# Performance work log

Hardware: AMD Instinct MI355X
Metric: run time of the kernel (lower is better)

Reference implementation:

```python
import jax, jax.numpy as jnp
import numpy as np

N, E, F_IN, F_E = 50000, 800000, 128, 16
R, H, C = 4, 4, 32            # num_relations, heads, out_channels
HC = H * C                     # 128
NEG_SLOPE = 0.2                # PyG RGATConv default negative_slope
EPS = 1e-16                    # PyG softmax epsilon


def rgat_conv(x, src, dst, edge_type, edge_attr, w, q, k, e, le, b, concat):
    """Faithful PyG RGATConv (additive-self-attention, across-relation, dim=1, aggr=add).
    x: [N,F]; w: [R,F,H*C]; q,k,e: [H*C,H]; le: [F_e,H*C]; b: bias."""
    n = x.shape[0]
    xw = jnp.einsum('nf,rfo->rno', x, w)              # [R,N,H*C] per-relation projections
    x_i = xw[edge_type, dst]                          # [E,H*C] target-node proj per edge
    x_j = xw[edge_type, src]                          # [E,H*C] source-node proj per edge
    qi = x_i @ q                                      # [E,H]
    kj = x_j @ k + (edge_attr @ le) @ e               # [E,H] (edge features folded into keys)
    alpha = jax.nn.leaky_relu(qi + kj, NEG_SLOPE)     # [E,H]
    # softmax over incoming edges of each destination node (across relations)
    amax = jax.ops.segment_max(alpha, dst, num_segments=n)
    ex = jnp.exp(alpha - amax[dst])
    denom = jax.ops.segment_sum(ex, dst, num_segments=n)
    alpha = ex / (denom[dst] + EPS)
    msg = alpha[:, :, None] * x_j.reshape(-1, H, C)   # [E,H,C]
    out = jax.ops.segment_sum(msg, dst, num_segments=n)  # [N,H,C] sum aggregation
    out = out.reshape(n, H * C) if concat else out.mean(axis=1)
    return out + b


def setup_inputs() -> dict:
    key = jax.random.key(0)
    ks = jax.random.split(key, 18)
    p = 0.05
    inp = {
        'x': jax.random.normal(ks[0], (N, F_IN), dtype=jnp.float32),
        'edge_index': jax.random.randint(ks[1], (2, E), 0, N, dtype=jnp.int64)
            if jax.config.jax_enable_x64 else jax.random.randint(ks[1], (2, E), 0, N).astype(jnp.int32),
        'edge_attr': jax.random.normal(ks[2], (E, F_E), dtype=jnp.float32),
        'edge_type': jax.random.randint(ks[3], (E,), 0, R).astype(jnp.int32),
        # conv1 params (in=F_IN, concat=True -> bias of size H*C)
        'w1': jax.random.normal(ks[4], (R, F_IN, HC), dtype=jnp.float32) * p,
        'q1': jax.random.normal(ks[5], (HC, H), dtype=jnp.float32) * p,
        'k1': jax.random.normal(ks[6], (HC, H), dtype=jnp.float32) * p,
        'e1': jax.random.normal(ks[7], (HC, H), dtype=jnp.float32) * p,
        'le1': jax.random.normal(ks[8], (F_E, HC), dtype=jnp.float32) * p,
        'b1': jnp.zeros((HC,), dtype=jnp.float32),
        # conv3 params (in=H*C=128, concat=False -> bias of size C)
        'w3': jax.random.normal(ks[9], (R, HC, HC), dtype=jnp.float32) * p,
        'q3': jax.random.normal(ks[10], (HC, H), dtype=jnp.float32) * p,
        'k3': jax.random.normal(ks[11], (HC, H), dtype=jnp.float32) * p,
        'e3': jax.random.normal(ks[12], (HC, H), dtype=jnp.float32) * p,
        'le3': jax.random.normal(ks[13], (F_E, HC), dtype=jnp.float32) * p,
        'b3': jnp.zeros((C,), dtype=jnp.float32),
    }
    return inp


def reference(x, edge_index, edge_attr, edge_type,
              w1, q1, k1, e1, le1, b1,
              w3, q3, k3, e3, le3, b3):
    src, dst = edge_index[0], edge_index[1]
    h = jax.nn.relu(rgat_conv(x, src, dst, edge_type, edge_attr,
                              w1, q1, k1, e1, le1, b1, concat=True))
    out = rgat_conv(h, src, dst, edge_type, edge_attr,
                    w3, q3, k3, e3, le3, b3, concat=False)
    return out
```

## Files before the change

### kernel.cpp

```cpp
#include <hip/hip_runtime.h>


#define NEG_SLOPE 0.2f
#define SOFT_EPS 1e-16f

typedef __attribute__((ext_vector_type(8))) short bf16x8;
typedef __attribute__((ext_vector_type(4))) float f32x4;
typedef __attribute__((ext_vector_type(4))) unsigned short u16x4;
typedef __attribute__((ext_vector_type(4))) _Float16 half4;
typedef __attribute__((ext_vector_type(8))) _Float16 half8;

__device__ __forceinline__ void bf16split(float f, unsigned short& h, unsigned short& l) {
  unsigned u = __float_as_uint(f);
  unsigned r = u + 0x7FFFu + ((u >> 16) & 1u);
  h = (unsigned short)(r >> 16);
  float fh = __uint_as_float(((unsigned)h) << 16);
  float d = f - fh;
  unsigned u2 = __float_as_uint(d);
  unsigned r2 = u2 + 0x7FFFu + ((u2 >> 16) & 1u);
  l = (unsigned short)(r2 >> 16);
}

__global__ void lee_kernel(const float* __restrict__ le1, const float* __restrict__ e1,
                           const float* __restrict__ le3, const float* __restrict__ e3,
                           float* __restrict__ lee) {
  int t = threadIdx.x;
  const float* le = (t < 64) ? le1 : le3;
  const float* ee = (t < 64) ? e1 : e3;
  int u = t & 63, f = u >> 2, h = u & 3;
  float acc = 0.f;
  for (int o = 0; o < 128; ++o) acc += le[f * 128 + o] * ee[o * 4 + h];
  lee[t] = acc;
}

__global__ __launch_bounds__(256) void wqk_kernel(
    const float* __restrict__ w1, const float* __restrict__ q1, const float* __restrict__ k1,
    const float* __restrict__ w3, const float* __restrict__ q3, const float* __restrict__ k3,
    float* __restrict__ wqk) {
  int idx = blockIdx.x * 256 + threadIdx.x;
  int L = idx >> 12, rem = idx & 4095;
  int r = rem >> 10, rem2 = rem & 1023, f = rem2 >> 3, j = rem2 & 7;
  const float* w = L ? w3 : w1;
  const float* qk = (j < 4) ? (L ? q3 : q1) : (L ? k3 : k1);
  int h = j & 3;
  const float* wrow = w + ((size_t)r * 128 + f) * 128;
  float acc = 0.f;
  for (int o = 0; o < 128; ++o) acc += wrow[o] * qk[o * 4 + h];
  wqk[idx] = acc;
}

__global__ __launch_bounds__(256) void hist_kernel(const int* __restrict__ dst,
                                                   int* __restrict__ deg, int E) {
  int e = blockIdx.x * 256 + threadIdx.x;
  if (e < E) atomicAdd(&deg[dst[e]], 1);
}

__global__ __launch_bounds__(256) void scanA_kernel(const int* __restrict__ deg,
                                                    int* __restrict__ bsum, int N) {
  int b = blockIdx.x, t = threadIdx.x;
  int base = b * 1024 + t * 4;
  int s = 0;
#pragma unroll
  for (int j = 0; j < 4; ++j) {
    int i = base + j;
    if (i < N) s += deg[i];
  }
#pragma unroll
  for (int o = 1; o < 64; o <<= 1) s += __shfl_xor(s, o);
  __shared__ int wsum[4];
  if ((t & 63) == 0) wsum[t >> 6] = s;
  __syncthreads();
  if (t == 0) bsum[b] = wsum[0] + wsum[1] + wsum[2] + wsum[3];
}

__global__ __launch_bounds__(256) void scanB_kernel(const int* __restrict__ bsum,
                                                    int* __restrict__ boff,
                                                    int* __restrict__ row_start,
                                                    int nb, int N) {
  int t = threadIdx.x;
  int v = (t < nb) ? bsum[t] : 0;
  int inc = v;
#pragma unroll
  for (int o = 1; o < 64; o <<= 1) {
    int u = __shfl_up(inc, o);
    if ((t & 63) >= o) inc += u;
  }
  __shared__ int wt[4];
  if ((t & 63) == 63) wt[t >> 6] = inc;
  __syncthreads();
  int add = 0;
  for (int wv = 0; wv < (t >> 6); ++wv) add += wt[wv];
  inc += add;
  if (t < nb) boff[t] = inc - v;
  if (t == 255) row_start[N] = inc;
}

__global__ __launch_bounds__(256) void scanC_kernel(const int* __restrict__ deg,
                                                    const int* __restrict__ boff,
                                                    int* __restrict__ row_start,
                                                    int* __restrict__ cursor, int N) {
  int b = blockIdx.x, t = threadIdx.x;
  int base = b * 1024 + t * 4;
  int d[4];
  int s = 0;
#pragma unroll
  for (int j = 0; j < 4; ++j) {
    int i = base + j;
    d[j] = (i < N) ? deg[i] : 0;
    s += d[j];
  }
  int inc = s;
#pragma unroll
  for (int o = 1; o < 64; o <<= 1) {
    int u = __shfl_up(inc, o);
    if ((t & 63) >= o) inc += u;
  }
  __shared__ int wt[4];
  if ((t & 63) == 63) wt[t >> 6] = inc;
  __syncthreads();
  int add = boff[b];
  for (int wv = 0; wv < (t >> 6); ++wv) add += wt[wv];
  int off = add + inc - s;
#pragma unroll
  for (int j = 0; j < 4; ++j) {
    int i = base + j;
    if (i < N) {
      row_start[i] = off;
      cursor[i] = off;
      off += d[j];
    }
  }
}

__global__ __launch_bounds__(256) void scatter_kernel(
    const int* __restrict__ src, const int* __restrict__ dst, const int* __restrict__ et,
    int* __restrict__ cursor, int4* __restrict__ es, int E) {
  int e = blockIdx.x * 256 + threadIdx.x;
  if (e >= E) return;
  int d = dst[e];
  int pos = atomicAdd(&cursor[d], 1);
  es[pos] = make_int4(src[e], d, et[e], e);
}

__global__ __launch_bounds__(256) void ek2_kernel(
    const int4* __restrict__ es, const float* __restrict__ ea,
    const float* __restrict__ lee, float* __restrict__ eks1,
    float* __restrict__ eks3, int E) {
  __shared__ float sl[128];
  if (threadIdx.x < 128) sl[threadIdx.x] = lee[threadIdx.x];
  __syncthreads();
  int i = blockIdx.x * 256 + threadIdx.x;
  if (i >= E) return;
  int eid = es[i].w;
  const float4* a4 = (const float4*)(ea + (size_t)eid * 16);
  float a1[4] = {0, 0, 0, 0}, a3[4] = {0, 0, 0, 0};
#pragma unroll
  for (int ii = 0; ii < 4; ++ii) {
    float4 v = a4[ii];
    int f = ii * 4;
#pragma unroll
    for (int h = 0; h < 4; ++h) {
      a1[h] += v.x * sl[f * 4 + h] + v.y * sl[(f + 1) * 4 + h] +
               v.z * sl[(f + 2) * 4 + h] + v.w * sl[(f + 3) * 4 + h];
      a3[h] += v.x * sl[64 + f * 4 + h] + v.y * sl[64 + (f + 1) * 4 + h] +
               v.z * sl[64 + (f + 2) * 4 + h] + v.w * sl[64 + (f + 3) * 4 + h];
    }
  }
  *(float4*)(eks1 + (size_t)i * 4) = make_float4(a1[0], a1[1], a1[2], a1[3]);
  *(float4*)(eks3 + (size_t)i * 4) = make_float4(a3[0], a3[1], a3[2], a3[3]);
}

__global__ __launch_bounds__(256) void convx_kernel(const float* __restrict__ in,
                                                    unsigned short* __restrict__ hi,
                                                    unsigned short* __restrict__ lo,
                                                    int total8) {
  int i = blockIdx.x * 256 + threadIdx.x;
  if (i >= total8) return;
  const float4* p = (const float4*)in + (size_t)i * 2;
  float4 a = p[0], b = p[1];
  float v[8] = {a.x, a.y, a.z, a.w, b.x, b.y, b.z, b.w};
  bf16x8 hv, lv;
#pragma unroll
  for (int j = 0; j < 8; ++j) {
    unsigned short h, l;
    bf16split(v[j], h, l);
    hv[j] = (short)h; lv[j] = (short)l;
  }
  *(bf16x8*)(hi + (size_t)i * 8) = hv;
  *(bf16x8*)(lo + (size_t)i * 8) = lv;
}

__global__ void convw_kernel(const float* __restrict__ w,
                             unsigned short* __restrict__ hiT,
                             unsigned short* __restrict__ loT) {
  int f = blockIdx.x, r = blockIdx.y, o = threadIdx.x;
  float v = w[((size_t)r * 128 + f) * 128 + o];
  unsigned short h, l;
  bf16split(v, h, l);
  hiT[((size_t)r * 128 + o) * 128 + f] = h;
  loT[((size_t)r * 128 + o) * 128 + f] = l;
}

__global__ __launch_bounds__(256) void proj_mfma_kernel(
    const unsigned short* __restrict__ xhi, const unsigned short* __restrict__ xlo,
    const unsigned short* __restrict__ whiT, const unsigned short* __restrict__ wloT,
    _Float16* __restrict__ xwh, int N) {
  __shared__ bf16x8 wl_h[2048];
  __shared__ bf16x8 wl_l[2048];
  int r = blockIdx.x;
  int nb = blockIdx.y * 128;
  int t = threadIdx.x;
  const unsigned short* wh = whiT + (size_t)r * (128 * 128);
  const unsigned short* wl = wloT + (size_t)r * (128 * 128);

#pragma unroll
  for (int j = 0; j < 8; ++j) {
    int i = j * 256 + t;
    int c = i & 15, q = (i >> 4) & 3, kc = (i >> 6) & 3, ot = i >> 8;
    int srco = (ot * 16 + c) * 128 + kc * 32 + q * 8;
    wl_h[i] = *(const bf16x8*)(wh + srco);
    wl_l[i] = *(const bf16x8*)(wl + srco);
  }
  __syncthreads();

  int wv = t >> 6;
  int lane = t & 63;
  int c = lane & 15, q = lane >> 4;
  int nodebase = nb + wv * 32;
  int n0 = nodebase + c;
  int n1 = nodebase + 16 + c;
  int n0c = n0 < N ? n0 : N - 1;
  int n1c = n1 < N ? n1 : N - 1;

  f32x4 acc[8][2];
#pragma unroll
  for (int ot = 0; ot < 8; ++ot)
#pragma unroll
    for (int nt = 0; nt < 2; ++nt) acc[ot][nt] = (f32x4){0.f, 0.f, 0.f, 0.f};

  bf16x8 xb[2][4];
  {
    int k0 = q * 8;
    xb[0][0] = *(const bf16x8*)(xhi + (size_t)n0c * 128 + k0);
    xb[0][1] = *(const bf16x8*)(xlo + (size_t)n0c * 128 + k0);
    xb[0][2] = *(const bf16x8*)(xhi + (size_t)n1c * 128 + k0);
    xb[0][3] = *(const bf16x8*)(xlo + (size_t)n1c * 128 + k0);
  }
#pragma unroll
  for (int kc = 0; kc < 4; ++kc) {
    if (kc < 3) {
      int k0 = (kc + 1) * 32 + q * 8;
      xb[(kc + 1) & 1][0] = *(const bf16x8*)(xhi + (size_t)n0c * 128 + k0);
      xb[(kc + 1) & 1][1] = *(const bf16x8*)(xlo + (size_t)n0c * 128 + k0);
      xb[(kc + 1) & 1][2] = *(const bf16x8*)(xhi + (size_t)n1c * 128 + k0);
      xb[(kc + 1) & 1][3] = *(const bf16x8*)(xlo + (size_t)n1c * 128 + k0);
    }
    bf16x8 b0h = xb[kc & 1][0], b0l = xb[kc & 1][1];
    bf16x8 b1h = xb[kc & 1][2], b1l = xb[kc & 1][3];
#pragma unroll
    for (int ot = 0; ot < 8; ++ot) {
      int fi = ((ot * 4 + kc) * 4 + q) * 16 + c;
      bf16x8 ah = wl_h[fi];
      bf16x8 al = wl_l[fi];
      acc[ot][0] = __builtin_amdgcn_mfma_f32_16x16x32_bf16(ah, b0h, acc[ot][0], 0, 0, 0);
      acc[ot][0] = __builtin_amdgcn_mfma_f32_16x16x32_bf16(ah, b0l, acc[ot][0], 0, 0, 0);
      acc[ot][0] = __builtin_amdgcn_mfma_f32_16x16x32_bf16(al, b0h, acc[ot][0], 0, 0, 0);
      acc[ot][1] = __builtin_amdgcn_mfma_f32_16x16x32_bf16(ah, b1h, acc[ot][1], 0, 0, 0);
      acc[ot][1] = __builtin_amdgcn_mfma_f32_16x16x32_bf16(ah, b1l, acc[ot][1], 0, 0, 0);
      acc[ot][1] = __builtin_amdgcn_mfma_f32_16x16x32_bf16(al, b1h, acc[ot][1], 0, 0, 0);
    }
  }

#pragma unroll
  for (int nt = 0; nt < 2; ++nt) {
    int n = nodebase + nt * 16 + c;
    if (n < N) {
      _Float16* basep = xwh + ((size_t)r * N + n) * 128 + q * 4;
#pragma unroll
      for (int ot = 0; ot < 8; ++ot) {
        f32x4 a = acc[ot][nt];
        half4 hv;
        hv[0] = (_Float16)a.x; hv[1] = (_Float16)a.y;
        hv[2] = (_Float16)a.z; hv[3] = (_Float16)a.w;
        *(half4*)(basep + ot * 16) = hv;
      }
    }
  }
}

__global__ __launch_bounds__(256) void qkx_kernel(
    const float* __restrict__ xin, const float* __restrict__ wqk,
    float* __restrict__ qn, float* __restrict__ kn, int N) {
  __shared__ float sx[64 * 132];
  __shared__ float swqk[4 * 1032];
  int nb = blockIdx.x * 64;
  int t = threadIdx.x;
#pragma unroll
  for (int j = 0; j < 16; ++j) {
    int i = j * 256 + t;
    swqk[(i >> 10) * 1032 + (i & 1023)] = wqk[i];
  }
#pragma unroll
  for (int j = 0; j < 8; ++j) {
    int i = j * 256 + t;
    int n = nb + (i >> 5); if (n >= N) n = N - 1;
    ((float4*)sx)[(i >> 5) * 33 + (i & 31)] =
        ((const float4*)(xin + (size_t)n * 128))[i & 31];
  }
  __syncthreads();
  int rl = t >> 2, r = t & 3;
  float aq0 = 0, aq1 = 0, aq2 = 0, aq3 = 0;
  float ak0 = 0, ak1 = 0, ak2 = 0, ak3 = 0;
  const float* xr = sx + rl * 132;
  const float* wb = swqk + r * 1032;
  for (int f = 0; f < 128; ++f) {
    float xv = xr[f];
    float4 qw = *(const float4*)(wb + f * 8);
    float4 kw = *(const float4*)(wb + f * 8 + 4);
    aq0 += xv * qw.x; aq1 += xv * qw.y; aq2 += xv * qw.z; aq3 += xv * qw.w;
    ak0 += xv * kw.x; ak1 += xv * kw.y; ak2 += xv * kw.z; ak3 += xv * kw.w;
  }
  int n = nb + rl;
  if (n < N) {
    *(float4*)(qn + ((size_t)r * N + n) * 4) = make_float4(aq0, aq1, aq2, aq3);
    *(float4*)(kn + ((size_t)r * N + n) * 4) = make_float4(ak0, ak1, ak2, ak3);
  }
}

__global__ __launch_bounds__(256) void agg_kernel(
    const int4* __restrict__ es, const int* __restrict__ row_start,
    const float* __restrict__ qn, const float* __restrict__ kn,
    const float* __restrict__ eks, float* __restrict__ alpha_s,
    const _Float16* __restrict__ xwh, const float* __restrict__ bias,
    float* __restrict__ out, unsigned short* __restrict__ xhi,
    unsigned short* __restrict__ xlo, int N, int concat) {
  int d = blockIdx.x * 4 + (threadIdx.x >> 6);
  if (d >= N) return;
  int lane = threadIdx.x & 63;
  int rs = row_start[d], re = row_start[d + 1];
  int deg = re - rs;

  float4 qv0 = *(const float4*)(qn + (size_t)d * 4);
  float4 qv1 = *(const float4*)(qn + ((size_t)N + d) * 4);
  float4 qv2 = *(const float4*)(qn + ((size_t)2 * N + d) * 4);
  float4 qv3 = *(const float4*)(qn + ((size_t)3 * N + d) * 4);

  float4 m = make_float4(-1e30f, -1e30f, -1e30f, -1e30f);
  float4 a_last = m;
  for (int i = rs + lane; i < re; i += 64) {
    int4 v = es[i];
    float4 kv = *(const float4*)(kn + ((size_t)v.z * N + v.x) * 4);
    float4 ev = *(const float4*)(eks + (size_t)i * 4);
    float4 q4 = (v.z == 0) ? qv0 : (v.z == 1) ? qv1 : (v.z == 2) ? qv2 : qv3;
    float4 a = make_float4(q4.x + kv.x + ev.x, q4.y + kv.y + ev.y,
                           q4.z + kv.z + ev.z, q4.w + kv.w + ev.w);
    a.x = a.x > 0.f ? a.x : NEG_SLOPE * a.x;
    a.y = a.y > 0.f ? a.y : NEG_SLOPE * a.y;
    a.z = a.z > 0.f ? a.z : NEG_SLOPE * a.z;
    a.w = a.w > 0.f ? a.w : NEG_SLOPE * a.w;
    if (deg > 64) ((float4*)alpha_s)[i] = a;
    m.x = fmaxf(m.x, a.x); m.y = fmaxf(m.y, a.y);
    m.z = fmaxf(m.z, a.z); m.w = fmaxf(m.w, a.w);
    a_last = a;
  }
#pragma unroll
  for (int o = 32; o >= 1; o >>= 1) {
    m.x = fmaxf(m.x, __shfl_xor(m.x, o));
    m.y = fmaxf(m.y, __shfl_xor(m.y, o));
    m.z = fmaxf(m.z, __shfl_xor(m.z, o));
    m.w = fmaxf(m.w, __shfl_xor(m.w, o));
  }
  float4 s = make_float4(0.f, 0.f, 0.f, 0.f);
  if (deg <= 64) {
    if (lane < deg) {
      float4 e4 = make_float4(__expf(a_last.x - m.x), __expf(a_last.y - m.y),
                              __expf(a_last.z - m.z), __expf(a_last.w - m.w));
      ((float4*)alpha_s)[rs + lane] = e4;
      s = e4;
    }
  } else {
    for (int i = rs + lane; i < re; i += 64) {
      float4 a = ((const float4*)alpha_s)[i];
      float4 e4 = make_float4(__expf(a.x - m.x), __expf(a.y - m.y),
                              __expf(a.z - m.z), __expf(a.w - m.w));
      ((float4*)alpha_s)[i] = e4;
      s.x += e4.x; s.y += e4.y; s.z += e4.z; s.w += e4.w;
    }
  }
#pragma unroll
  for (int o = 32; o >= 1; o >>= 1) {
    s.x += __shfl_xor(s.x, o); s.y += __shfl_xor(s.y, o);
    s.z += __shfl_xor(s.z, o); s.w += __shfl_xor(s.w, o);
  }

  int quar = lane >> 4;
  int cl = lane & 15;
  int h = cl >> 2;
  float smh = (h == 0) ? s.x : (h == 1) ? s.y : (h == 2) ? s.z : s.w;
  float rden = 1.f / (smh + SOFT_EPS);

  float acc[8];
#pragma unroll
  for (int j = 0; j < 8; ++j) acc[j] = 0.f;
  int base = rs;
  for (; base + 8 <= re; base += 8) {
    int e0 = base + quar, e1 = base + 4 + quar;
    int4 a0 = es[e0];
    int4 a1 = es[e1];
    float w0 = alpha_s[(size_t)e0 * 4 + h];
    float w1 = alpha_s[(size_t)e1 * 4 + h];
    half8 x0 = *(const half8*)(xwh + ((size_t)a0.z * N + a0.x) * 128 + cl * 8);
    half8 x1 = *(const half8*)(xwh + ((size_t)a1.z * N + a1.x) * 128 + cl * 8);
#pragma unroll
    for (int j = 0; j < 8; ++j) {
      acc[j] = fmaf((float)x0[j], w0, acc[j]);
      acc[j] = fmaf((float)x1[j], w1, acc[j]);
    }
  }
  for (; base < re; base += 4) {
    int e = base + quar;
    if (e < re) {
      int4 a = es[e];
      float w = alpha_s[(size_t)e * 4 + h];
      half8 xv = *(const half8*)(xwh + ((size_t)a.z * N + a.x) * 128 + cl * 8);
#pragma unroll
      for (int j = 0; j < 8; ++j) acc[j] = fmaf((float)xv[j], w, acc[j]);
    }
  }
#pragma unroll
  for (int j = 0; j < 8; ++j) {
    acc[j] += __shfl_xor(acc[j], 16);
    acc[j] += __shfl_xor(acc[j], 32);
    acc[j] *= rden;
  }

  if (concat) {
    if (quar == 0) {
      float4 b0 = ((const float4*)bias)[cl * 2];
      float4 b1 = ((const float4*)bias)[cl * 2 + 1];
      float v[8] = {acc[0] + b0.x, acc[1] + b0.y, acc[2] + b0.z, acc[3] + b0.w,
                    acc[4] + b1.x, acc[5] + b1.y, acc[6] + b1.z, acc[7] + b1.w};
      u16x4 hv0, lv0, hv1, lv1;
#pragma unroll
      for (int j = 0; j < 8; ++j) {
        v[j] = v[j] > 0.f ? v[j] : 0.f;
        unsigned short hh, ll;
        bf16split(v[j], hh, ll);
        if (j < 4) { hv0[j] = hh; lv0[j] = ll; }
        else { hv1[j - 4] = hh; lv1[j - 4] = ll; }
      }
      float* orow = out + (size_t)d * 128 + cl * 8;
      *(float4*)orow = make_float4(v[0], v[1], v[2], v[3]);
      *(float4*)(orow + 4) = make_float4(v[4], v[5], v[6], v[7]);
      *(u16x4*)(xhi + (size_t)d * 128 + cl * 8) = hv0;
      *(u16x4*)(xhi + (size_t)d * 128 + cl * 8 + 4) = hv1;
      *(u16x4*)(xlo + (size_t)d * 128 + cl * 8) = lv0;
      *(u16x4*)(xlo + (size_t)d * 128 + cl * 8 + 4) = lv1;
    }
  } else {
#pragma unroll
    for (int j = 0; j < 8; ++j) {
      acc[j] += __shfl_xor(acc[j], 4);
      acc[j] += __shfl_xor(acc[j], 8);
    }
    if (lane < 4) {
      float4 b0 = ((const float4*)bias)[cl * 2];
      float4 b1 = ((const float4*)bias)[cl * 2 + 1];
      float* orow = out + (size_t)d * 32 + cl * 8;
      *(float4*)orow = make_float4(0.25f * acc[0] + b0.x, 0.25f * acc[1] + b0.y,
                                   0.25f * acc[2] + b0.z, 0.25f * acc[3] + b0.w);
      *(float4*)(orow + 4) = make_float4(0.25f * acc[4] + b1.x, 0.25f * acc[5] + b1.y,
                                         0.25f * acc[6] + b1.z, 0.25f * acc[7] + b1.w);
    }
  }
}

extern "C" void kernel_launch(void* const* d_in, const int* in_sizes, int n_in,
                              void* d_out, int out_size, void* d_ws, size_t ws_size,
                              hipStream_t stream) {
  const float* x   = (const float*)d_in[0];
  const int*   ei  = (const int*)d_in[1];
  const float* ea  = (const float*)d_in[2];
  const int*   etp = (const int*)d_in[3];
  const float* w1  = (const float*)d_in[4];
  const float* q1  = (const float*)d_in[5];
  const float* k1  = (const float*)d_in[6];
  const float* e1  = (const float*)d_in[7];
  const float* le1 = (const float*)d_in[8];
  const float* b1  = (const float*)d_in[9];
  const float* w3  = (const float*)d_in[10];
  const float* q3  = (const float*)d_in[11];
  const float* k3  = (const float*)d_in[12];
  const float* e3  = (const float*)d_in[13];
  const float* le3 = (const float*)d_in[14];
  const float* b3  = (const float*)d_in[15];
  const int N = in_sizes[0] / 128;
  const int E = in_sizes[3];
  const int* srcp = ei;
  const int* dstp = ei + E;

  float* ws   = (float*)d_ws;
  _Float16* xwh = (_Float16*)ws;
  float* qn   = ws + (size_t)2 * N * 128;
  float* kn   = qn + (size_t)4 * N * 4;
  float* eks1 = kn + (size_t)4 * N * 4;
  float* eks3 = eks1 + (size_t)E * 4;
  float* alph = eks3 + (size_t)E * 4;
  float* hbuf = alph + (size_t)E * 4;
  float* leeb = hbuf + (size_t)N * 128;
  float* wqkb = leeb + 128;
  int* deg      = (int*)(wqkb + 8192);
  int* rowst    = deg + N;
  int* cursor   = rowst + N + 1;
  int* bsum     = cursor + N;
  int* boff     = bsum + 256;
  uintptr_t pe = (uintptr_t)(boff + 256);
  pe = (pe + 15) & ~(uintptr_t)15;
  int4* es      = (int4*)pe;
  uintptr_t pa = (uintptr_t)(es + E);
  pa = (pa + 255) & ~(uintptr_t)255;
  unsigned short* xhi  = (unsigned short*)pa;
  unsigned short* xlo  = xhi + (size_t)N * 128;
  unsigned short* whiT = xlo + (size_t)N * 128;
  unsigned short* wloT = whiT + 4 * 128 * 128;
  (void)ws_size; (void)n_in; (void)out_size;

  int eb   = (E + 255) / 256;
  int nb4  = (N + 3) / 4;
  int nbs  = (N + 1023) / 1024;
  int pgy  = (N + 127) / 128;
  int qxb  = (N + 63) / 64;
  int cxb  = (N * 128 / 8 + 255) / 256;

  hipMemsetAsync(deg, 0, (size_t)N * sizeof(int), stream);
  hist_kernel<<<eb, 256, 0, stream>>>(dstp, deg, E);
  scanA_kernel<<<nbs, 256, 0, stream>>>(deg, bsum, N);
  scanB_kernel<<<1, 256, 0, stream>>>(bsum, boff, rowst, nbs, N);
  scanC_kernel<<<nbs, 256, 0, stream>>>(deg, boff, rowst, cursor, N);
  scatter_kernel<<<eb, 256, 0, stream>>>(srcp, dstp, etp, cursor, es, E);
  lee_kernel<<<1, 128, 0, stream>>>(le1, e1, le3, e3, leeb);
  ek2_kernel<<<eb, 256, 0, stream>>>(es, ea, leeb, eks1, eks3, E);
  wqk_kernel<<<32, 256, 0, stream>>>(w1, q1, k1, w3, q3, k3, wqkb);
  convx_kernel<<<cxb, 256, 0, stream>>>(x, xhi, xlo, N * 128 / 8);

  for (int layer = 0; layer < 2; ++layer) {
    const float* xin = layer ? hbuf : x;
    const float* w   = layer ? w3 : w1;
    const float* eks = layer ? eks3 : eks1;
    const float* bias = layer ? b3 : b1;
    float* outp = layer ? (float*)d_out : hbuf;

    convw_kernel<<<dim3(128, 4), 128, 0, stream>>>(w, whiT, wloT);
    proj_mfma_kernel<<<dim3(4, pgy), 256, 0, stream>>>(xhi, xlo, whiT, wloT, xwh, N);
    qkx_kernel<<<qxb, 256, 0, stream>>>(xin, wqkb + layer * 4096, qn, kn, N);
    agg_kernel<<<nb4, 256, 0, stream>>>(es, rowst, qn, kn, eks, alph, xwh,
                                        bias, outp, xhi, xlo, N, layer == 0 ? 1 : 0);
  }
}
```

Measured before the change: 489.7 us.

## Map one destination node per 16-lane group in aggregation kernel

Reassigns agg_kernel from one 64-lane wavefront per destination node to one 16-lane group per node, so four nodes share a wavefront. Average in-degree is about 16, so the old mapping left most lanes idle in the softmax phase and spent cross-lane reductions on them. The gather loop now has each lane handle 8 channels across all edges serially, which removes the cross-quarter shuffle reduction. In exchange, per-lane serial work grows, lanes with different node degrees diverge within a wavefront, and index arithmetic moves from size_t to int, which risks overflow on larger graphs.

```diff
diff --git a/kernel.cpp b/kernel.cpp
--- a/kernel.cpp
+++ b/kernel.cpp
@@ -327,6 +327,24 @@
   }
 }
 
+__device__ __forceinline__ float4 edge_alpha(const int4* __restrict__ es,
+                                             const float* __restrict__ qn,
+                                             const float* __restrict__ kn,
+                                             const float* __restrict__ eks,
+                                             int i, int d, int N) {
+  int4 v = es[i];
+  float4 kv = *(const float4*)(kn + (v.z * N + v.x) * 4);
+  float4 ev = ((const float4*)eks)[i];
+  float4 q4 = *(const float4*)(qn + (v.z * N + d) * 4);
+  float4 a = make_float4(q4.x + kv.x + ev.x, q4.y + kv.y + ev.y,
+                         q4.z + kv.z + ev.z, q4.w + kv.w + ev.w);
+  a.x = a.x > 0.f ? a.x : NEG_SLOPE * a.x;
+  a.y = a.y > 0.f ? a.y : NEG_SLOPE * a.y;
+  a.z = a.z > 0.f ? a.z : NEG_SLOPE * a.z;
+  a.w = a.w > 0.f ? a.w : NEG_SLOPE * a.w;
+  return a;
+}
+
 __global__ __launch_bounds__(256) void agg_kernel(
     const int4* __restrict__ es, const int* __restrict__ row_start,
     const float* __restrict__ qn, const float* __restrict__ kn,
@@ -334,52 +352,60 @@
     const _Float16* __restrict__ xwh, const float* __restrict__ bias,
     float* __restrict__ out, unsigned short* __restrict__ xhi,
     unsigned short* __restrict__ xlo, int N, int concat) {
-  int d = blockIdx.x * 4 + (threadIdx.x >> 6);
+  int d = blockIdx.x * 16 + (threadIdx.x >> 4);
   if (d >= N) return;
-  int lane = threadIdx.x & 63;
+  int ql = threadIdx.x & 15;
   int rs = row_start[d], re = row_start[d + 1];
   int deg = re - rs;
-
-  float4 qv0 = *(const float4*)(qn + (size_t)d * 4);
-  float4 qv1 = *(const float4*)(qn + ((size_t)N + d) * 4);
-  float4 qv2 = *(const float4*)(qn + ((size_t)2 * N + d) * 4);
-  float4 qv3 = *(const float4*)(qn + ((size_t)3 * N + d) * 4);
+  bool fast = (deg <= 64);
 
   float4 m = make_float4(-1e30f, -1e30f, -1e30f, -1e30f);
-  float4 a_last = m;
-  for (int i = rs + lane; i < re; i += 64) {
-    int4 v = es[i];
-    float4 kv = *(const float4*)(kn + ((size_t)v.z * N + v.x) * 4);
-    float4 ev = *(const float4*)(eks + (size_t)i * 4);
-    float4 q4 = (v.z == 0) ? qv0 : (v.z == 1) ? qv1 : (v.z == 2) ? qv2 : qv3;
-    float4 a = make_float4(q4.x + kv.x + ev.x, q4.y + kv.y + ev.y,
-                           q4.z + kv.z + ev.z, q4.w + kv.w + ev.w);
-    a.x = a.x > 0.f ? a.x : NEG_SLOPE * a.x;
-    a.y = a.y > 0.f ? a.y : NEG_SLOPE * a.y;
-    a.z = a.z > 0.f ? a.z : NEG_SLOPE * a.z;
-    a.w = a.w > 0.f ? a.w : NEG_SLOPE * a.w;
-    if (deg > 64) ((float4*)alpha_s)[i] = a;
-    m.x = fmaxf(m.x, a.x); m.y = fmaxf(m.y, a.y);
-    m.z = fmaxf(m.z, a.z); m.w = fmaxf(m.w, a.w);
-    a_last = a;
-  }
-#pragma unroll
-  for (int o = 32; o >= 1; o >>= 1) {
+  float4 ar0 = m, ar1 = m, ar2 = m, ar3 = m;
+  if (fast) {
+#define SWEEPA(IT, AR)                                              \
+    if (IT * 16 + ql < deg) {                                       \
+      float4 a = edge_alpha(es, qn, kn, eks, rs + IT * 16 + ql, d, N); \
+      AR = a;                                                       \
+      m.x = fmaxf(m.x, a.x); m.y = fmaxf(m.y, a.y);                 \
+      m.z = fmaxf(m.z, a.z); m.w = fmaxf(m.w, a.w);                 \
+    }
+    SWEEPA(0, ar0)
+    SWEEPA(1, ar1)
+    SWEEPA(2, ar2)
+    SWEEPA(3, ar3)
+#undef SWEEPA
+  } else {
+    for (int i = rs + ql; i < re; i += 16) {
+      float4 a = edge_alpha(es, qn, kn, eks, i, d, N);
+      ((float4*)alpha_s)[i] = a;
+      m.x = fmaxf(m.x, a.x); m.y = fmaxf(m.y, a.y);
+      m.z = fmaxf(m.z, a.z); m.w = fmaxf(m.w, a.w);
+    }
+  }
+#pragma unroll
+  for (int o = 1; o < 16; o <<= 1) {
     m.x = fmaxf(m.x, __shfl_xor(m.x, o));
     m.y = fmaxf(m.y, __shfl_xor(m.y, o));
     m.z = fmaxf(m.z, __shfl_xor(m.z, o));
     m.w = fmaxf(m.w, __shfl_xor(m.w, o));
   }
+
   float4 s = make_float4(0.f, 0.f, 0.f, 0.f);
-  if (deg <= 64) {
-    if (lane < deg) {
-      float4 e4 = make_float4(__expf(a_last.x - m.x), __expf(a_last.y - m.y),
-                              __expf(a_last.z - m.z), __expf(a_last.w - m.w));
-      ((float4*)alpha_s)[rs + lane] = e4;
-      s = e4;
-    }
+  if (fast) {
+#define SWEEPB(IT, AR)                                                       \
+    if (IT * 16 + ql < deg) {                                                \
+      float4 e4 = make_float4(__expf(AR.x - m.x), __expf(AR.y - m.y),        \
+                              __expf(AR.z - m.z), __expf(AR.w - m.w));       \
+      ((float4*)alpha_s)[rs + IT * 16 + ql] = e4;                            \
+      s.x += e4.x; s.y += e4.y; s.z += e4.z; s.w += e4.w;                    \
+    }
+    SWEEPB(0, ar0)
+    SWEEPB(1, ar1)
+    SWEEPB(2, ar2)
+    SWEEPB(3, ar3)
+#undef SWEEPB
   } else {
-    for (int i = rs + lane; i < re; i += 64) {
+    for (int i = rs + ql; i < re; i += 16) {
       float4 a = ((const float4*)alpha_s)[i];
       float4 e4 = make_float4(__expf(a.x - m.x), __expf(a.y - m.y),
                               __expf(a.z - m.z), __expf(a.w - m.w));
@@ -388,85 +414,73 @@
     }
   }
 #pragma unroll
-  for (int o = 32; o >= 1; o >>= 1) {
+  for (int o = 1; o < 16; o <<= 1) {
     s.x += __shfl_xor(s.x, o); s.y += __shfl_xor(s.y, o);
     s.z += __shfl_xor(s.z, o); s.w += __shfl_xor(s.w, o);
   }
 
-  int quar = lane >> 4;
-  int cl = lane & 15;
-  int h = cl >> 2;
+  int h = ql >> 2;
   float smh = (h == 0) ? s.x : (h == 1) ? s.y : (h == 2) ? s.z : s.w;
   float rden = 1.f / (smh + SOFT_EPS);
 
   float acc[8];
 #pragma unroll
   for (int j = 0; j < 8; ++j) acc[j] = 0.f;
-  int base = rs;
-  for (; base + 8 <= re; base += 8) {
-    int e0 = base + quar, e1 = base + 4 + quar;
-    int4 a0 = es[e0];
-    int4 a1 = es[e1];
-    float w0 = alpha_s[(size_t)e0 * 4 + h];
-    float w1 = alpha_s[(size_t)e1 * 4 + h];
-    half8 x0 = *(const half8*)(xwh + ((size_t)a0.z * N + a0.x) * 128 + cl * 8);
-    half8 x1 = *(const half8*)(xwh + ((size_t)a1.z * N + a1.x) * 128 + cl * 8);
+  int e = rs;
+  for (; e + 2 <= re; e += 2) {
+    int4 a0 = es[e];
+    int4 a1 = es[e + 1];
+    float w0 = alpha_s[e * 4 + h];
+    float w1 = alpha_s[(e + 1) * 4 + h];
+    half8 x0 = *(const half8*)(xwh + (a0.z * N + a0.x) * 128 + ql * 8);
+    half8 x1 = *(const half8*)(xwh + (a1.z * N + a1.x) * 128 + ql * 8);
 #pragma unroll
     for (int j = 0; j < 8; ++j) {
       acc[j] = fmaf((float)x0[j], w0, acc[j]);
       acc[j] = fmaf((float)x1[j], w1, acc[j]);
     }
   }
-  for (; base < re; base += 4) {
-    int e = base + quar;
-    if (e < re) {
-      int4 a = es[e];
-      float w = alpha_s[(size_t)e * 4 + h];
-      half8 xv = *(const half8*)(xwh + ((size_t)a.z * N + a.x) * 128 + cl * 8);
-#pragma unroll
-      for (int j = 0; j < 8; ++j) acc[j] = fmaf((float)xv[j], w, acc[j]);
-    }
-  }
-#pragma unroll
-  for (int j = 0; j < 8; ++j) {
-    acc[j] += __shfl_xor(acc[j], 16);
-    acc[j] += __shfl_xor(acc[j], 32);
-    acc[j] *= rden;
-  }
+  if (e < re) {
+    int4 a0 = es[e];
+    float w0 = alpha_s[e * 4 + h];
+    half8 x0 = *(const half8*)(xwh + (a0.z * N + a0.x) * 128 + ql * 8);
+#pragma unroll
+    for (int j = 0; j < 8; ++j) acc[j] = fmaf((float)x0[j], w0, acc[j]);
+  }
+#pragma unroll
+  for (int j = 0; j < 8; ++j) acc[j] *= rden;
 
   if (concat) {
-    if (quar == 0) {
-      float4 b0 = ((const float4*)bias)[cl * 2];
-      float4 b1 = ((const float4*)bias)[cl * 2 + 1];
-      float v[8] = {acc[0] + b0.x, acc[1] + b0.y, acc[2] + b0.z, acc[3] + b0.w,
-                    acc[4] + b1.x, acc[5] + b1.y, acc[6] + b1.z, acc[7] + b1.w};
-      u16x4 hv0, lv0, hv1, lv1;
-#pragma unroll
-      for (int j = 0; j < 8; ++j) {
-        v[j] = v[j] > 0.f ? v[j] : 0.f;
-        unsigned short hh, ll;
-        bf16split(v[j], hh, ll);
-        if (j < 4) { hv0[j] = hh; lv0[j] = ll; }
-        else { hv1[j - 4] = hh; lv1[j - 4] = ll; }
-      }
-      float* orow = out + (size_t)d * 128 + cl * 8;
-      *(float4*)orow = make_float4(v[0], v[1], v[2], v[3]);
-      *(float4*)(orow + 4) = make_float4(v[4], v[5], v[6], v[7]);
-      *(u16x4*)(xhi + (size_t)d * 128 + cl * 8) = hv0;
-      *(u16x4*)(xhi + (size_t)d * 128 + cl * 8 + 4) = hv1;
-      *(u16x4*)(xlo + (size_t)d * 128 + cl * 8) = lv0;
-      *(u16x4*)(xlo + (size_t)d * 128 + cl * 8 + 4) = lv1;
-    }
+    float4 b0 = ((const float4*)bias)[ql * 2];
+    float4 b1 = ((const float4*)bias)[ql * 2 + 1];
+    float v[8] = {acc[0] + b0.x, acc[1] + b0.y, acc[2] + b0.z, acc[3] + b0.w,
+                  acc[4] + b1.x, acc[5] + b1.y, acc[6] + b1.z, acc[7] + b1.w};
+    u16x4 hv0, lv0, hv1, lv1;
+#pragma unroll
+    for (int j = 0; j < 8; ++j) {
+      v[j] = v[j] > 0.f ? v[j] : 0.f;
+      unsigned short hh, ll;
+      bf16split(v[j], hh, ll);
+      if (j < 4) { hv0[j] = hh; lv0[j] = ll; }
+      else { hv1[j - 4] = hh; lv1[j - 4] = ll; }
+    }
+    float* orow = out + (size_t)d * 128 + ql * 8;
+    *(float4*)orow = make_float4(v[0], v[1], v[2], v[3]);
+    *(float4*)(orow + 4) = make_float4(v[4], v[5], v[6], v[7]);
+    *(u16x4*)(xhi + (size_t)d * 128 + ql * 8) = hv0;
+    *(u16x4*)(xhi + (size_t)d * 128 + ql * 8 + 4) = hv1;
+    *(u16x4*)(xlo + (size_t)d * 128 + ql * 8) = lv0;
+    *(u16x4*)(xlo + (size_t)d * 128 + ql * 8 + 4) = lv1;
   } else {
 #pragma unroll
     for (int j = 0; j < 8; ++j) {
       acc[j] += __shfl_xor(acc[j], 4);
       acc[j] += __shfl_xor(acc[j], 8);
     }
-    if (lane < 4) {
-      float4 b0 = ((const float4*)bias)[cl * 2];
-      float4 b1 = ((const float4*)bias)[cl * 2 + 1];
-      float* orow = out + (size_t)d * 32 + cl * 8;
+    if (ql < 4) {
+      float4 b0 = ((const float4*)bias)[ql * 2];
+      float4 b1 = ((const float4*)bias)[ql * 2 + 1];
+      float* orow = out + (size_t)d * 32 + ql * 8;
       *(float4*)orow = make_float4(0.25f * acc[0] + b0.x, 0.25f * acc[1] + b0.y,
                                    0.25f * acc[2] + b0.z, 0.25f * acc[3] + b0.w);
       *(float4*)(orow + 4) = make_float4(0.25f * acc[4] + b1.x, 0.25f * acc[5] + b1.y,
@@ -526,7 +540,7 @@
   (void)ws_size; (void)n_in; (void)out_size;
 
   int eb   = (E + 255) / 256;
-  int nb4  = (N + 3) / 4;
+  int nb16 = (N + 15) / 16;
   int nbs  = (N + 1023) / 1024;
   int pgy  = (N + 127) / 128;
   int qxb  = (N + 63) / 64;
@@ -553,7 +567,7 @@
     convw_kernel<<<dim3(128, 4), 128, 0, stream>>>(w, whiT, wloT);
     proj_mfma_kernel<<<dim3(4, pgy), 256, 0, stream>>>(xhi, xlo, whiT, wloT, xwh, N);
     qkx_kernel<<<qxb, 256, 0, stream>>>(xin, wqkb + layer * 4096, qn, kn, N);
-    agg_kernel<<<nb4, 256, 0, stream>>>(es, rowst, qn, kn, eks, alph, xwh,
-                                        bias, outp, xhi, xlo, N, layer == 0 ? 1 : 0);
-  }
-}
+    agg_kernel<<<nb16, 256, 0, stream>>>(es, rowst, qn, kn, eks, xwh == 0 ? alph : alph, xwh,
+                                         bias, outp, xhi, xlo, N, layer == 0 ? 1 : 0);
+  }
+}
```

Result: no change. 496.5 us (+1.4%).
